# Performance work log

Measured on AMD Instinct MI355X. Metric: run time of the kernel, lower is better.

## Reference

```python
import jax, jax.numpy as jnp
import numpy as np

N_SPARSE, N_SEQ, N_DENSE = 16, 2, 13
VOCAB, EMBED_DIM, SEQ_LEN = 100000, 64, 50
BATCH = 4096


def setup_inputs() -> dict:
    key = jax.random.key(0)
    k1, k2, k3, k4, k5 = jax.random.split(key, 5)
    return {
        "sparse_tables": jax.random.normal(k1, (N_SPARSE, VOCAB, EMBED_DIM), dtype=jnp.float32),
        "seq_tables": jax.random.normal(k2, (N_SEQ, VOCAB, EMBED_DIM), dtype=jnp.float32),
        "dense_vals": jax.random.normal(k3, (BATCH, N_DENSE), dtype=jnp.float32),
        "sparse_idx": jax.random.randint(k4, (N_SPARSE, BATCH), 0, VOCAB, dtype=jnp.int32),
        "seq_idx": jax.random.randint(k5, (N_SEQ, BATCH, SEQ_LEN), 0, VOCAB, dtype=jnp.int32),
    }


def reference(sparse_tables, seq_tables, dense_vals, sparse_idx, seq_idx):
    # Per-feature gather for sparse features: [F, B, D] -> [B, F, D]
    sparse_emb = jax.vmap(lambda tab, idx: tab[idx])(sparse_tables, sparse_idx)
    sparse_emb = jnp.transpose(sparse_emb, (1, 0, 2))  # [B, N_SPARSE, D]

    # Sequence feature gathers: [N_SEQ, B, S, D]
    seq_emb = jax.vmap(lambda tab, idx: tab[idx])(seq_tables, seq_idx)

    # Feature 0: SumPooling -> [B, D]
    sum_pooled = jnp.sum(seq_emb[0], axis=1)

    # Feature 1: AveragePooling (divide per embed-dim by count of nonzero
    # embedding values along seq, exactly as the torch module does)
    e = seq_emb[1]  # [B, S, D]
    non_padding = jnp.sum((e != 0).astype(jnp.float32), axis=1)  # [B, D]
    mean_pooled = jnp.sum(e, axis=1) / (non_padding + 1e-16)

    # Concat along feature axis then flatten (squeeze_dim=True path)
    all_emb = jnp.concatenate(
        [sparse_emb, sum_pooled[:, None, :], mean_pooled[:, None, :]], axis=1
    )  # [B, N_SPARSE + N_SEQ, D]
    flat = all_emb.reshape(all_emb.shape[0], -1)
    return jnp.concatenate([flat, dense_vals], axis=1)  # [B, 18*64 + 13]
```

## Files before the change

### kernel.cpp

```cpp
#include <hip/hip_runtime.h>

#define N_SPARSE 16
#define N_SEQ    2
#define N_DENSE  13
#define VOCAB    100000
#define EMBED    64
#define SEQ_LEN  50
#define BATCH    4096
#define N_FEAT   (N_SPARSE + N_SEQ)
#define OUT_COLS (N_FEAT * EMBED + N_DENSE)

#define SEQ_WAVES (N_SEQ * BATCH)
#define SB_WAVES  (BATCH)
#define TOT_WAVES (SEQ_WAVES + SB_WAVES)
#define NBLOCKS   (TOT_WAVES / 4)

__global__ __launch_bounds__(256) void emb_kernel(
    const float* __restrict__ sparse_tables,
    const float* __restrict__ seq_tables,
    const float* __restrict__ dense_vals,
    const int* __restrict__ sparse_idx,
    const int* __restrict__ seq_idx,
    float* __restrict__ out)
{
    const int w    = blockIdx.x * 4 + (threadIdx.x >> 6);
    const int lane = threadIdx.x & 63;
    const int g    = lane >> 4;
    const int l16  = lane & 15;

    if (w < SEQ_WAVES) {
        const int sf = w >> 12;
        const int b  = w & (BATCH - 1);
        const int* ip = seq_idx + ((size_t)(sf * BATCH + b)) * SEQ_LEN;
        int myidx = (lane < SEQ_LEN) ? ip[lane] : 0;
        const float* tab = seq_tables + (size_t)sf * VOCAB * EMBED;

        float ax = 0.f, ay = 0.f, az = 0.f, aw = 0.f;
        float cx = 0.f, cy = 0.f, cz = 0.f, cw = 0.f;

        #pragma unroll
        for (int i = 0; i < 12; ++i) {
            const int row = i * 4 + g;
            const int idx = __shfl(myidx, row);
            const float4 v = *reinterpret_cast<const float4*>(
                tab + (size_t)idx * EMBED + 4 * l16);
            ax += v.x; ay += v.y; az += v.z; aw += v.w;
            cx += (v.x != 0.f) ? 1.f : 0.f;
            cy += (v.y != 0.f) ? 1.f : 0.f;
            cz += (v.z != 0.f) ? 1.f : 0.f;
            cw += (v.w != 0.f) ? 1.f : 0.f;
        }
        {
            const int row = 48 + g;
            const int idx = __shfl(myidx, (row < SEQ_LEN) ? row : 0);
            if (row < SEQ_LEN) {
                const float4 v = *reinterpret_cast<const float4*>(
                    tab + (size_t)idx * EMBED + 4 * l16);
                ax += v.x; ay += v.y; az += v.z; aw += v.w;
                cx += (v.x != 0.f) ? 1.f : 0.f;
                cy += (v.y != 0.f) ? 1.f : 0.f;
                cz += (v.z != 0.f) ? 1.f : 0.f;
                cw += (v.w != 0.f) ? 1.f : 0.f;
            }
        }

        ax += __shfl_xor(ax, 16); ax += __shfl_xor(ax, 32);
        ay += __shfl_xor(ay, 16); ay += __shfl_xor(ay, 32);
        az += __shfl_xor(az, 16); az += __shfl_xor(az, 32);
        aw += __shfl_xor(aw, 16); aw += __shfl_xor(aw, 32);
        if (sf == 1) {
            cx += __shfl_xor(cx, 16); cx += __shfl_xor(cx, 32);
            cy += __shfl_xor(cy, 16); cy += __shfl_xor(cy, 32);
            cz += __shfl_xor(cz, 16); cz += __shfl_xor(cz, 32);
            cw += __shfl_xor(cw, 16); cw += __shfl_xor(cw, 32);
            ax = ax / (cx + 1e-16f);
            ay = ay / (cy + 1e-16f);
            az = az / (cz + 1e-16f);
            aw = aw / (cw + 1e-16f);
        }

        if (lane < 16) {
            float* o = out + (size_t)b * OUT_COLS + (N_SPARSE + sf) * EMBED + 4 * l16;
            o[0] = ax; o[1] = ay; o[2] = az; o[3] = aw;
        }
    } else {
        const int b = w - SEQ_WAVES;
        int myidx16 = (lane < N_SPARSE) ? sparse_idx[lane * BATCH + b] : 0;

        float4 v[4];
        #pragma unroll
        for (int i = 0; i < 4; ++i) {
            const int f   = i * 4 + g;
            const int idx = __shfl(myidx16, f);
            v[i] = *reinterpret_cast<const float4*>(
                sparse_tables + ((size_t)f * VOCAB + idx) * EMBED + 4 * l16);
        }
        float* ob = out + (size_t)b * OUT_COLS;
        #pragma unroll
        for (int i = 0; i < 4; ++i) {
            const int f = i * 4 + g;
            float* o = ob + f * EMBED + 4 * l16;
            o[0] = v[i].x; o[1] = v[i].y; o[2] = v[i].z; o[3] = v[i].w;
        }
        if (lane < N_DENSE)
            ob[N_FEAT * EMBED + lane] = dense_vals[b * N_DENSE + lane];
    }
}

extern "C" void kernel_launch(void* const* d_in, const int* in_sizes, int n_in,
                              void* d_out, int out_size, void* d_ws, size_t ws_size,
                              hipStream_t stream) {
    const float* sparse_tables = (const float*)d_in[0];
    const float* seq_tables    = (const float*)d_in[1];
    const float* dense_vals    = (const float*)d_in[2];
    const int*   sparse_idx    = (const int*)d_in[3];
    const int*   seq_idx       = (const int*)d_in[4];
    float*       out           = (float*)d_out;

    emb_kernel<<<dim3(NBLOCKS), dim3(256), 0, stream>>>(
        sparse_tables, seq_tables, dense_vals, sparse_idx, seq_idx, out);
}
```

Before: 480.6 us.

## Split each sequence row across two waves per block and batch gathers

New measurement: 483.8 us. No clear change (+0.7%).

```diff
diff --git a/kernel.cpp b/kernel.cpp
--- a/kernel.cpp
+++ b/kernel.cpp
@@ -10,10 +10,11 @@
 #define N_FEAT   (N_SPARSE + N_SEQ)
 #define OUT_COLS (N_FEAT * EMBED + N_DENSE)
 
-#define SEQ_WAVES (N_SEQ * BATCH)
-#define SB_WAVES  (BATCH)
-#define TOT_WAVES (SEQ_WAVES + SB_WAVES)
-#define NBLOCKS   (TOT_WAVES / 4)
+typedef float f4v __attribute__((ext_vector_type(4)));
+
+#define SEQ_BLOCKS BATCH
+#define SB_BLOCKS  (BATCH / 4)
+#define NBLOCKS    (SEQ_BLOCKS + SB_BLOCKS)
 
 __global__ __launch_bounds__(256) void emb_kernel(
     const float* __restrict__ sparse_tables,
@@ -23,77 +24,90 @@
     const int* __restrict__ seq_idx,
     float* __restrict__ out)
 {
-    const int w    = blockIdx.x * 4 + (threadIdx.x >> 6);
-    const int lane = threadIdx.x & 63;
+    const int tid  = threadIdx.x;
+    const int lane = tid & 63;
+    const int wv   = tid >> 6;
     const int g    = lane >> 4;
     const int l16  = lane & 15;
 
-    if (w < SEQ_WAVES) {
-        const int sf = w >> 12;
-        const int b  = w & (BATCH - 1);
+    if (blockIdx.x < SEQ_BLOCKS) {
+        __shared__ float s_sum[4][EMBED];
+        __shared__ float s_cnt[4][EMBED];
+
+        const int b  = blockIdx.x;
+        const int sf = wv >> 1;
+        const int h  = wv & 1;
+
         const int* ip = seq_idx + ((size_t)(sf * BATCH + b)) * SEQ_LEN;
         int myidx = (lane < SEQ_LEN) ? ip[lane] : 0;
         const float* tab = seq_tables + (size_t)sf * VOCAB * EMBED;
 
+        int ridx[7];
+        #pragma unroll
+        for (int i = 0; i < 7; ++i)
+            ridx[i] = __shfl(myidx, h * 25 + i * 4 + g);
+
+        float4 v[7];
+        #pragma unroll
+        for (int i = 0; i < 7; ++i) {
+            const int rl = i * 4 + g;
+            if (rl < 25)
+                v[i] = *reinterpret_cast<const float4*>(
+                    tab + (size_t)ridx[i] * EMBED + 4 * l16);
+            else
+                v[i] = make_float4(0.f, 0.f, 0.f, 0.f);
+        }
+
         float ax = 0.f, ay = 0.f, az = 0.f, aw = 0.f;
         float cx = 0.f, cy = 0.f, cz = 0.f, cw = 0.f;
-
         #pragma unroll
-        for (int i = 0; i < 12; ++i) {
-            const int row = i * 4 + g;
-            const int idx = __shfl(myidx, row);
-            const float4 v = *reinterpret_cast<const float4*>(
-                tab + (size_t)idx * EMBED + 4 * l16);
-            ax += v.x; ay += v.y; az += v.z; aw += v.w;
-            cx += (v.x != 0.f) ? 1.f : 0.f;
-            cy += (v.y != 0.f) ? 1.f : 0.f;
-            cz += (v.z != 0.f) ? 1.f : 0.f;
-            cw += (v.w != 0.f) ? 1.f : 0.f;
-        }
-        {
-            const int row = 48 + g;
-            const int idx = __shfl(myidx, (row < SEQ_LEN) ? row : 0);
-            if (row < SEQ_LEN) {
-                const float4 v = *reinterpret_cast<const float4*>(
-                    tab + (size_t)idx * EMBED + 4 * l16);
-                ax += v.x; ay += v.y; az += v.z; aw += v.w;
-                cx += (v.x != 0.f) ? 1.f : 0.f;
-                cy += (v.y != 0.f) ? 1.f : 0.f;
-                cz += (v.z != 0.f) ? 1.f : 0.f;
-                cw += (v.w != 0.f) ? 1.f : 0.f;
-            }
+        for (int i = 0; i < 7; ++i) {
+            ax += v[i].x; ay += v[i].y; az += v[i].z; aw += v[i].w;
+            cx += (v[i].x != 0.f) ? 1.f : 0.f;
+            cy += (v[i].y != 0.f) ? 1.f : 0.f;
+            cz += (v[i].z != 0.f) ? 1.f : 0.f;
+            cw += (v[i].w != 0.f) ? 1.f : 0.f;
         }
 
         ax += __shfl_xor(ax, 16); ax += __shfl_xor(ax, 32);
         ay += __shfl_xor(ay, 16); ay += __shfl_xor(ay, 32);
         az += __shfl_xor(az, 16); az += __shfl_xor(az, 32);
         aw += __shfl_xor(aw, 16); aw += __shfl_xor(aw, 32);
-        if (sf == 1) {
-            cx += __shfl_xor(cx, 16); cx += __shfl_xor(cx, 32);
-            cy += __shfl_xor(cy, 16); cy += __shfl_xor(cy, 32);
-            cz += __shfl_xor(cz, 16); cz += __shfl_xor(cz, 32);
-            cw += __shfl_xor(cw, 16); cw += __shfl_xor(cw, 32);
-            ax = ax / (cx + 1e-16f);
-            ay = ay / (cy + 1e-16f);
-            az = az / (cz + 1e-16f);
-            aw = aw / (cw + 1e-16f);
-        }
+        cx += __shfl_xor(cx, 16); cx += __shfl_xor(cx, 32);
+        cy += __shfl_xor(cy, 16); cy += __shfl_xor(cy, 32);
+        cz += __shfl_xor(cz, 16); cz += __shfl_xor(cz, 32);
+        cw += __shfl_xor(cw, 16); cw += __shfl_xor(cw, 32);
 
         if (lane < 16) {
-            float* o = out + (size_t)b * OUT_COLS + (N_SPARSE + sf) * EMBED + 4 * l16;
-            o[0] = ax; o[1] = ay; o[2] = az; o[3] = aw;
+            float4* ss = reinterpret_cast<float4*>(&s_sum[wv][4 * l16]);
+            float4* sc = reinterpret_cast<float4*>(&s_cnt[wv][4 * l16]);
+            *ss = make_float4(ax, ay, az, aw);
+            *sc = make_float4(cx, cy, cz, cw);
+        }
+        __syncthreads();
+
+        if (tid < 2 * EMBED) {
+            const int osf = tid >> 6;
+            const int c   = tid & 63;
+            float s = s_sum[2 * osf][c] + s_sum[2 * osf + 1][c];
+            if (osf == 1) {
+                const float cnt = s_cnt[2][c] + s_cnt[3][c];
+                s = s / (cnt + 1e-16f);
+            }
+            out[(size_t)b * OUT_COLS + (N_SPARSE + osf) * EMBED + c] = s;
         }
     } else {
-        const int b = w - SEQ_WAVES;
+        const int b = (blockIdx.x - SEQ_BLOCKS) * 4 + wv;
         int myidx16 = (lane < N_SPARSE) ? sparse_idx[lane * BATCH + b] : 0;
 
-        float4 v[4];
+        f4v v[4];
         #pragma unroll
         for (int i = 0; i < 4; ++i) {
             const int f   = i * 4 + g;
             const int idx = __shfl(myidx16, f);
-            v[i] = *reinterpret_cast<const float4*>(
-                sparse_tables + ((size_t)f * VOCAB + idx) * EMBED + 4 * l16);
+            v[i] = __builtin_nontemporal_load(
+                reinterpret_cast<const f4v*>(
+                    sparse_tables + ((size_t)f * VOCAB + idx) * EMBED + 4 * l16));
         }
         float* ob = out + (size_t)b * OUT_COLS;
         #pragma unroll
```
